# Optimization experiments

Hardware: AMD Instinct MI355X
Metric: run time of the kernel (lower is better)

The kernel has to match this reference:

```python
import jax, jax.numpy as jnp
import numpy as np

N_HEAD = 8
DIM_K = 64
DIM_MODEL = N_HEAD * DIM_K  # 512; must equal seq_len for the final batch_dot
SCALE = DIM_K ** 0.5


def setup_inputs() -> dict:
    key = jax.random.key(0)
    ks = jax.random.split(key, 4)
    B, S, D_IN = 32, 512, 128
    x = jax.random.normal(ks[0], (B, S, D_IN), dtype=jnp.float32)
    init = 0.02
    Wq = jax.random.normal(ks[1], (D_IN * N_HEAD, DIM_MODEL), dtype=jnp.float32) * init
    Wk = jax.random.normal(ks[2], (D_IN * N_HEAD, DIM_MODEL), dtype=jnp.float32) * init
    Wv = jax.random.normal(ks[3], (D_IN * N_HEAD, DIM_MODEL), dtype=jnp.float32) * init
    z = jnp.zeros((DIM_MODEL,), dtype=jnp.float32)
    return {"x": x, "Wq": Wq, "bq": z, "Wk": Wk, "bk": z, "Wv": Wv, "bv": z}


def reference(x, Wq, bq, Wk, bk, Wv, bv):
    # Tile input n_head times along feature dim (matches K.concatenate([q]*n_head))
    xt = jnp.concatenate([x] * N_HEAD, axis=-1)          # [B, S, d_in*n_head]
    q = xt @ Wq + bq                                      # [B, S, dim_model]
    k = xt @ Wk + bk
    v = xt @ Wv + bv
    # K.batch_dot(q, k, axes=[-1,-1]) -> q @ k^T per batch
    scores = jnp.einsum('bsd,btd->bst', q, k) / SCALE     # [B, S, S]
    attn = jax.nn.softmax(scores, axis=-1)
    # K.batch_dot(v, attn, axes=[2,-1]): out[b,i,j] = sum_k v[b,i,k]*attn[b,j,k]
    # (only valid because S == dim_model, as in the original buggy layer)
    out = jnp.einsum('bik,bjk->bij', v, attn)             # [B, S, S]
    return out
```

## Files before the change

### kernel.cpp

```cpp
#include <hip/hip_runtime.h>


typedef unsigned short u16;
typedef __attribute__((ext_vector_type(8))) short bf16x8;
typedef __attribute__((ext_vector_type(4))) float f32x4;
typedef __attribute__((ext_vector_type(2))) float f32x2;
typedef __attribute__((ext_vector_type(2))) unsigned int u32x2;

__device__ inline u16 f2bf(float f) {
  unsigned u = __float_as_uint(f);
  u = u + 0x7fffu + ((u >> 16) & 1u);
  return (u16)(u >> 16);
}
__device__ inline float bf2f(u16 h) { return __uint_as_float(((unsigned)h) << 16); }

__device__ inline void gl16(const u16* g, u16* l) {
  __builtin_amdgcn_global_load_lds(
      (const __attribute__((address_space(1))) unsigned int*)g,
      (__attribute__((address_space(3))) unsigned int*)l, 16, 0, 0);
}

__global__ __launch_bounds__(256)
void prep_w(const float* __restrict__ Wq, const float* __restrict__ Wk,
            const float* __restrict__ Wv,
            u16* __restrict__ WTh, u16* __restrict__ WTl) {
  __shared__ float sm[128][17];
  int t  = blockIdx.x >> 5;
  int nb = blockIdx.x & 31;
  const float* W = (t == 0) ? Wq : (t == 1) ? Wk : Wv;
  int n0 = nb << 4;
  int nl = threadIdx.x & 15;
  int kq = threadIdx.x >> 4;
  float s[8];
#pragma unroll
  for (int i = 0; i < 8; ++i) s[i] = 0.f;
#pragma unroll
  for (int h = 0; h < 8; ++h)
#pragma unroll
    for (int i = 0; i < 8; ++i)
      s[i] += W[(h * 128 + kq + (i << 4)) * 512 + n0 + nl];
#pragma unroll
  for (int i = 0; i < 8; ++i) sm[kq + (i << 4)][nl] = s[i];
  __syncthreads();
  int no = threadIdx.x >> 4;
  int k8 = (threadIdx.x & 15) << 3;
  bf16x8 h8, l8;
#pragma unroll
  for (int c = 0; c < 8; ++c) {
    float v = sm[k8 + c][no];
    u16 h = f2bf(v);
    h8[c] = (short)h;
    l8[c] = (short)f2bf(v - bf2f(h));
  }
  long o = (long)t * 65536 + (long)(n0 + no) * 128 + k8;
  *(bf16x8*)&WTh[o] = h8;
  *(bf16x8*)&WTl[o] = l8;
}

__global__ __launch_bounds__(256)
void split_x(const float* __restrict__ x, u16* __restrict__ xh, u16* __restrict__ xl) {
  int i = blockIdx.x * 256 + threadIdx.x;
  const f32x4* xx = (const f32x4*)x;
  f32x4 a = xx[i * 2], b = xx[i * 2 + 1];
  float v[8] = {a[0], a[1], a[2], a[3], b[0], b[1], b[2], b[3]};
  bf16x8 h8, l8;
#pragma unroll
  for (int j = 0; j < 8; ++j) {
    u16 h = f2bf(v[j]);
    h8[j] = (short)h;
    l8[j] = (short)f2bf(v[j] - bf2f(h));
  }
  ((bf16x8*)xh)[i] = h8;
  ((bf16x8*)xl)[i] = l8;
}

__global__ __launch_bounds__(256, 2)
void proj_fused(const u16* __restrict__ xh, const u16* __restrict__ xl,
                const u16* __restrict__ WTh, const u16* __restrict__ WTl,
                u16* __restrict__ Qh, u16* __restrict__ Kh, u16* __restrict__ Vh,
                const float* __restrict__ bq, const float* __restrict__ bk,
                const float* __restrict__ bv) {
  __shared__ __align__(16) char ldsraw[65536];
  u16* st = (u16*)ldsraw;

  int tid = threadIdx.x;
  int bid = blockIdx.x;
  bid = (bid & 7) * 192 + (bid >> 3);
  int which = bid % 3;
  int tile  = bid / 3;
  int mt = tile >> 2;
  int nt = tile & 3;

  const u16* Ah = xh + (long)mt * (128 * 128);
  const u16* Al = xl + (long)mt * (128 * 128);
  const u16* Bh = WTh + which * 65536 + nt * 16384;
  const u16* Bl = WTl + which * 65536 + nt * 16384;
  const float* bias = (which == 0) ? bq : (which == 1) ? bk : bv;
  u16* C = (which == 0) ? Qh : (which == 1) ? Kh : Vh;

  int lane = tid & 63;
  int wv = tid >> 6;
  int wm = (wv >> 1) << 6;
  int wn = (wv & 1) << 6;
  int frow = lane & 15;
  int fk = (lane >> 4) << 3;

  f32x4 acc[4][4];
#pragma unroll
  for (int i = 0; i < 4; ++i)
#pragma unroll
    for (int j = 0; j < 4; ++j) {
      f32x4 z = {0.f, 0.f, 0.f, 0.f};
      acc[i][j] = z;
    }

  for (int kk = 0; kk < 2; ++kk) {
    int k0 = kk << 6;
#pragma unroll
    for (int j = 0; j < 4; ++j) {
      int c = j * 256 + tid;
      int row = c >> 3;
      int scol = ((c & 7) ^ (row & 7)) << 3;
      int ga = row * 128 + k0 + scol;
      int lo = c << 3;
      gl16(Ah + ga, st + lo);
      gl16(Al + ga, st + 8192 + lo);
      gl16(Bh + ga, st + 16384 + lo);
      gl16(Bl + ga, st + 24576 + lo);
    }
    __syncthreads();
#pragma unroll
    for (int ks = 0; ks < 2; ++ks) {
      int kb = (ks << 5) + fk;
      bf16x8 a_h[4], a_l[4], b_h[4], b_l[4];
#pragma unroll
      for (int i = 0; i < 4; ++i) {
        int ar = wm + (i << 4) + frow;
        int ao = ar * 64 + (kb ^ ((ar & 7) << 3));
        a_h[i] = *(const bf16x8*)&st[ao];
        a_l[i] = *(const bf16x8*)&st[8192 + ao];
        int br = wn + (i << 4) + frow;
        int bo = br * 64 + (kb ^ ((br & 7) << 3));
        b_h[i] = *(const bf16x8*)&st[16384 + bo];
        b_l[i] = *(const bf16x8*)&st[24576 + bo];
      }
#pragma unroll
      for (int i = 0; i < 4; ++i)
#pragma unroll
        for (int j = 0; j < 4; ++j) {
          acc[i][j] = __builtin_amdgcn_mfma_f32_16x16x32_bf16(a_h[i], b_h[j], acc[i][j], 0, 0, 0);
          acc[i][j] = __builtin_amdgcn_mfma_f32_16x16x32_bf16(a_l[i], b_h[j], acc[i][j], 0, 0, 0);
          acc[i][j] = __builtin_amdgcn_mfma_f32_16x16x32_bf16(a_h[i], b_l[j], acc[i][j], 0, 0, 0);
        }
    }
    __syncthreads();
  }

  float* tr = ((float*)ldsraw) + wv * 2112;
  int lr = lane >> 3;
  int c8 = (lane & 7) << 3;
  int colbase = (nt << 7) + wn + c8;
  float bb[8];
#pragma unroll
  for (int c = 0; c < 8; ++c) bb[c] = bias[colbase + c];
  long rowg0 = (long)(mt << 7) + wm;
#pragma unroll
  for (int q = 0; q < 2; ++q) {
#pragma unroll
    for (int il = 0; il < 2; ++il) {
      int i = (q << 1) + il;
#pragma unroll
      for (int j = 0; j < 4; ++j)
#pragma unroll
        for (int r = 0; r < 4; ++r)
          tr[((il << 4) + ((lane >> 4) << 2) + r) * 66 + (j << 4) + (lane & 15)] =
              acc[i][j][r];
    }
#pragma unroll
    for (int p = 0; p < 4; ++p) {
      int rr = (p << 3) + lr;
      float v[8];
      *(f32x2*)&v[0] = *(const f32x2*)&tr[rr * 66 + c8];
      *(f32x2*)&v[2] = *(const f32x2*)&tr[rr * 66 + c8 + 2];
      *(f32x2*)&v[4] = *(const f32x2*)&tr[rr * 66 + c8 + 4];
      *(f32x2*)&v[6] = *(const f32x2*)&tr[rr * 66 + c8 + 6];
      bf16x8 o8;
#pragma unroll
      for (int c = 0; c < 8; ++c) o8[c] = (short)f2bf(v[c] + bb[c]);
      *(bf16x8*)&C[(rowg0 + (q << 5) + rr) * 512 + colbase] = o8;
    }
  }
}

__global__ __launch_bounds__(512, 1)
void attn_fused(const u16* __restrict__ Q, const u16* __restrict__ K,
                const u16* __restrict__ V, float* __restrict__ OUT) {
  __shared__ __align__(16) char LDS[151552];
  u16* B0  = (u16*)LDS;
  u16* B1  = (u16*)(LDS + 32768);
  u16* P16 = (u16*)(LDS + 65536);
  u16* QB0 = (u16*)(LDS + 131072);
  u16* QB1 = (u16*)(LDS + 139264);
  float* smax = (float*)(LDS + 147456);
  float* ssum = (float*)(LDS + 149504);

  int tid = threadIdx.x;
  int p = blockIdx.x;
  int xcd = p & 7, sq = p >> 3;
  int b  = (xcd << 2) + (sq >> 3);
  int jb = sq & 7;

  const u16* Qp = Q + ((long)b * 512 + jb * 64) * 512;
  const u16* Kp = K + (long)b * 262144;
  const u16* Vp = V + (long)b * 262144;

  int lane = tid & 63, nw = tid >> 6;
  int frow = lane & 15, hi4 = lane >> 4;

  auto stageKV = [&](const u16* src, int h, int k0, u16* buf) {
#pragma unroll
    for (int j = 0; j < 4; ++j) {
      int u = (j << 9) + tid;
      int row = u >> 3, slot = u & 7;
      gl16(src + (long)((h << 8) + row) * 512 + k0 + ((slot ^ (row & 7)) << 3),
           buf + (u << 3));
    }
  };
  auto stageQ = [&](int k0, u16* qb) {
    int row = tid >> 3, slot = tid & 7;
    gl16(Qp + (long)row * 512 + k0 + ((slot ^ (row & 7)) << 3), qb + (tid << 3));
  };
  auto rf = [&](const u16* base, int R, int s) -> bf16x8 {
    return *(const bf16x8*)&base[(R << 6) + ((s ^ (R & 7)) << 3)];
  };

  f32x4 acc0[2][4], acc1[2][4];
#pragma unroll
  for (int jj = 0; jj < 2; ++jj)
#pragma unroll
    for (int ii = 0; ii < 4; ++ii) {
      f32x4 z = {0.f, 0.f, 0.f, 0.f};
      acc0[jj][ii] = z;
      acc1[jj][ii] = z;
    }

  stageKV(Kp, 0, 0, B0);
  stageQ(0, QB0);
  __syncthreads();

  for (int k = 0; k < 8; ++k) {
    int k0 = k << 6;
    const u16* qc = (k & 1) ? QB1 : QB0;
    stageKV(Kp, 1, k0, B1);
    {
      bf16x8 af[2][2], qf[2][4];
#pragma unroll
      for (int ks = 0; ks < 2; ++ks) {
#pragma unroll
        for (int jj = 0; jj < 2; ++jj)
          af[ks][jj] = rf(B0, (nw << 5) + (jj << 4) + frow, (ks << 2) + hi4);
#pragma unroll
        for (int ii = 0; ii < 4; ++ii)
          qf[ks][ii] = rf(qc, (ii << 4) + frow, (ks << 2) + hi4);
      }
      __builtin_amdgcn_s_setprio(1);
#pragma unroll
      for (int ks = 0; ks < 2; ++ks)
#pragma unroll
        for (int jj = 0; jj < 2; ++jj)
#pragma unroll
          for (int ii = 0; ii < 4; ++ii)
            acc0[jj][ii] = __builtin_amdgcn_mfma_f32_16x16x32_bf16(af[ks][jj], qf[ks][ii], acc0[jj][ii], 0, 0, 0);
      __builtin_amdgcn_s_setprio(0);
    }
    __syncthreads();
    if (k < 7) { stageKV(Kp, 0, k0 + 64, B0); stageQ(k0 + 64, (k & 1) ? QB0 : QB1); }
    else stageKV(Vp, 0, 0, B0);
    {
      bf16x8 af[2][2], qf[2][4];
#pragma unroll
      for (int ks = 0; ks < 2; ++ks) {
#pragma unroll
        for (int jj = 0; jj < 2; ++jj)
          af[ks][jj] = rf(B1, (nw << 5) + (jj << 4) + frow, (ks << 2) + hi4);
#pragma unroll
        for (int ii = 0; ii < 4; ++ii)
          qf[ks][ii] = rf(qc, (ii << 4) + frow, (ks << 2) + hi4);
      }
      __builtin_amdgcn_s_setprio(1);
#pragma unroll
      for (int ks = 0; ks < 2; ++ks)
#pragma unroll
        for (int jj = 0; jj < 2; ++jj)
#pragma unroll
          for (int ii = 0; ii < 4; ++ii)
            acc1[jj][ii] = __builtin_amdgcn_mfma_f32_16x16x32_bf16(af[ks][jj], qf[ks][ii], acc1[jj][ii], 0, 0, 0);
      __builtin_amdgcn_s_setprio(0);
    }
    if (k < 7) __syncthreads();
  }

  float mx[4], sm[4], inv_[4];
#pragma unroll
  for (int ii = 0; ii < 4; ++ii) {
    float m = acc0[0][ii][0];
#pragma unroll
    for (int jj = 0; jj < 2; ++jj)
#pragma unroll
      for (int r = 0; r < 4; ++r) {
        m = fmaxf(m, acc0[jj][ii][r]);
        m = fmaxf(m, acc1[jj][ii][r]);
      }
    m = fmaxf(m, __shfl_xor(m, 16));
    m = fmaxf(m, __shfl_xor(m, 32));
    mx[ii] = m;
  }
  __syncthreads();
  if (hi4 == 0) {
#pragma unroll
    for (int ii = 0; ii < 4; ++ii) smax[(((ii << 4) + frow) << 3) + nw] = mx[ii];
  }
  __syncthreads();
#pragma unroll
  for (int ii = 0; ii < 4; ++ii) {
    f32x4 a = *(const f32x4*)&smax[((ii << 4) + frow) << 3];
    f32x4 c = *(const f32x4*)&smax[(((ii << 4) + frow) << 3) + 4];
    mx[ii] = fmaxf(fmaxf(fmaxf(a[0], a[1]), fmaxf(a[2], a[3])),
                   fmaxf(fmaxf(c[0], c[1]), fmaxf(c[2], c[3])));
    sm[ii] = 0.f;
  }
#pragma unroll
  for (int jj = 0; jj < 2; ++jj)
#pragma unroll
    for (int ii = 0; ii < 4; ++ii)
#pragma unroll
      for (int r = 0; r < 4; ++r) {
        float p0 = __expf((acc0[jj][ii][r] - mx[ii]) * 0.125f);
        float p1 = __expf((acc1[jj][ii][r] - mx[ii]) * 0.125f);
        acc0[jj][ii][r] = p0;
        acc1[jj][ii][r] = p1;
        sm[ii] += p0 + p1;
      }
#pragma unroll
  for (int ii = 0; ii < 4; ++ii) {
    sm[ii] += __shfl_xor(sm[ii], 16);
    sm[ii] += __shfl_xor(sm[ii], 32);
  }
  if (hi4 == 0) {
#pragma unroll
    for (int ii = 0; ii < 4; ++ii) ssum[(((ii << 4) + frow) << 3) + nw] = sm[ii];
  }
  __syncthreads();
#pragma unroll
  for (int ii = 0; ii < 4; ++ii) {
    f32x4 a = *(const f32x4*)&ssum[((ii << 4) + frow) << 3];
    f32x4 c = *(const f32x4*)&ssum[(((ii << 4) + frow) << 3) + 4];
    inv_[ii] = 1.f / (a[0] + a[1] + a[2] + a[3] + c[0] + c[1] + c[2] + c[3]);
  }
#pragma unroll
  for (int ii = 0; ii < 4; ++ii) {
    int qr = (ii << 4) + frow;
    int rowoff = qr << 10;
    int swz = (qr & 7) << 4;
#pragma unroll
    for (int jj = 0; jj < 2; ++jj) {
      int c0 = ((nw << 5) + (jj << 4) + (hi4 << 2)) << 1;
      unsigned lo0 = (unsigned)f2bf(acc0[jj][ii][0] * inv_[ii]) |
                     ((unsigned)f2bf(acc0[jj][ii][1] * inv_[ii]) << 16);
      unsigned hi0 = (unsigned)f2bf(acc0[jj][ii][2] * inv_[ii]) |
                     ((unsigned)f2bf(acc0[jj][ii][3] * inv_[ii]) << 16);
      u32x2 w0 = {lo0, hi0};
      *(u32x2*)(LDS + 65536 + ((rowoff + c0) ^ swz)) = w0;
      unsigned lo1 = (unsigned)f2bf(acc1[jj][ii][0] * inv_[ii]) |
                     ((unsigned)f2bf(acc1[jj][ii][1] * inv_[ii]) << 16);
      unsigned hi1 = (unsigned)f2bf(acc1[jj][ii][2] * inv_[ii]) |
                     ((unsigned)f2bf(acc1[jj][ii][3] * inv_[ii]) << 16);
      u32x2 w1 = {lo1, hi1};
      *(u32x2*)(LDS + 65536 + ((rowoff + 512 + c0) ^ swz)) = w1;
    }
  }
  __syncthreads();

  f32x4 o0[2][4], o1[2][4];
#pragma unroll
  for (int jj = 0; jj < 2; ++jj)
#pragma unroll
    for (int ii = 0; ii < 4; ++ii) {
      f32x4 z = {0.f, 0.f, 0.f, 0.f};
      o0[jj][ii] = z;
      o1[jj][ii] = z;
    }

  for (int k = 0; k < 8; ++k) {
    int k0 = k << 6;
    stageKV(Vp, 1, k0, B1);
    {
      bf16x8 vf[2][2], pf[2][4];
#pragma unroll
      for (int ks = 0; ks < 2; ++ks) {
#pragma unroll
        for (int jj = 0; jj < 2; ++jj)
          vf[ks][jj] = rf(B0, (nw << 5) + (jj << 4) + frow, (ks << 2) + hi4);
#pragma unroll
        for (int ii = 0; ii < 4; ++ii) {
          int qr = (ii << 4) + frow;
          pf[ks][ii] = *(const bf16x8*)&P16[((qr << 9) + k0 + (ks << 5) + (hi4 << 3)) ^ ((qr & 7) << 3)];
        }
      }
      __builtin_amdgcn_s_setprio(1);
#pragma unroll
      for (int ks = 0; ks < 2; ++ks)
#pragma unroll
        for (int jj = 0; jj < 2; ++jj)
#pragma unroll
          for (int ii = 0; ii < 4; ++ii)
            o0[jj][ii] = __builtin_amdgcn_mfma_f32_16x16x32_bf16(vf[ks][jj], pf[ks][ii], o0[jj][ii], 0, 0, 0);
      __builtin_amdgcn_s_setprio(0);
    }
    __syncthreads();
    if (k < 7) stageKV(Vp, 0, k0 + 64, B0);
    {
      bf16x8 vf[2][2], pf[2][4];
#pragma unroll
      for (int ks = 0; ks < 2; ++ks) {
#pragma unroll
        for (int jj = 0; jj < 2; ++jj)
          vf[ks][jj] = rf(B1, (nw << 5) + (jj << 4) + frow, (ks << 2) + hi4);
#pragma unroll
        for (int ii = 0; ii < 4; ++ii) {
          int qr = (ii << 4) + frow;
          pf[ks][ii] = *(const bf16x8*)&P16[((qr << 9) + k0 + (ks << 5) + (hi4 << 3)) ^ ((qr & 7) << 3)];
        }
      }
      __builtin_amdgcn_s_setprio(1);
#pragma unroll
      for (int ks = 0; ks < 2; ++ks)
#pragma unroll
        for (int jj = 0; jj < 2; ++jj)
#pragma unroll
          for (int ii = 0; ii < 4; ++ii)
            o1[jj][ii] = __builtin_amdgcn_mfma_f32_16x16x32_bf16(vf[ks][jj], pf[ks][ii], o1[jj][ii], 0, 0, 0);
      __builtin_amdgcn_s_setprio(0);
    }
    if (k < 7) __syncthreads();
  }

  float* Ob = OUT + (long)b * 262144 + jb * 64;
#pragma unroll
  for (int jj = 0; jj < 2; ++jj)
#pragma unroll
    for (int ii = 0; ii < 4; ++ii)
#pragma unroll
      for (int r = 0; r < 4; ++r) {
        int vr = (nw << 5) + (jj << 4) + (hi4 << 2) + r;
        int qc = (ii << 4) + frow;
        Ob[(long)vr * 512 + qc] = o0[jj][ii][r];
        Ob[(long)(vr + 256) * 512 + qc] = o1[jj][ii][r];
      }
}

extern "C" void kernel_launch(void* const* d_in, const int* in_sizes, int n_in,
                              void* d_out, int out_size, void* d_ws, size_t ws_size,
                              hipStream_t stream) {
  const float* x  = (const float*)d_in[0];
  const float* Wq = (const float*)d_in[1];
  const float* bq = (const float*)d_in[2];
  const float* Wk = (const float*)d_in[3];
  const float* bk = (const float*)d_in[4];
  const float* Wv = (const float*)d_in[5];
  const float* bv = (const float*)d_in[6];
  float* out = (float*)d_out;

  char* ws = (char*)d_ws;
  size_t off = 0;
  auto alloc = [&](size_t bytes) -> char* {
    char* p = ws + off;
    off = (off + bytes + 255) & ~(size_t)255;
    return p;
  };
  u16* WTh = (u16*)alloc((size_t)3 * 512 * 128 * 2);
  u16* WTl = (u16*)alloc((size_t)3 * 512 * 128 * 2);
  u16* xh  = (u16*)alloc((size_t)16384 * 128 * 2);
  u16* xl  = (u16*)alloc((size_t)16384 * 128 * 2);
  u16* Qh  = (u16*)alloc((size_t)16384 * 512 * 2);
  u16* Kh  = (u16*)alloc((size_t)16384 * 512 * 2);
  u16* Vh  = (u16*)alloc((size_t)16384 * 512 * 2);

  prep_w<<<96, 256, 0, stream>>>(Wq, Wk, Wv, WTh, WTl);
  split_x<<<1024, 256, 0, stream>>>(x, xh, xl);
  proj_fused<<<1536, 256, 0, stream>>>(xh, xl, WTh, WTl, Qh, Kh, Vh, bq, bk, bv);
  attn_fused<<<256, 512, 0, stream>>>(Qh, Kh, Vh, out);
}
```

Before: 82.17 us.

## Preload full Q tile into LDS and use counted vmcnt waits with raw barriers

Loads the block's whole 64x512 Q tile into LDS once at the start, replacing per-step double-buffered Q staging, and reuses that region later for the P matrix. Replaces __syncthreads with explicit s_waitcnt vmcnt(4) plus s_barrier and sched_barrier, so the next K/V tile's loads can stay in flight while the current tile is consumed. Hoists the Q and P fragment reads ahead of the stage issue. The goal is less barrier and full-drain wait overhead and a smaller LDS footprint. The hand-counted vmcnt values and the aliasing of Q with P add correctness risk if the counts or ordering are wrong.

```diff
diff --git a/kernel.cpp b/kernel.cpp
--- a/kernel.cpp
+++ b/kernel.cpp
@@ -19,6 +19,11 @@
       (const __attribute__((address_space(1))) unsigned int*)g,
       (__attribute__((address_space(3))) unsigned int*)l, 16, 0, 0);
 }
+
+#define VM4  asm volatile("s_waitcnt vmcnt(4)" ::: "memory")
+#define VM0  asm volatile("s_waitcnt vmcnt(0)" ::: "memory")
+#define RBAR __builtin_amdgcn_s_barrier()
+#define SB0  __builtin_amdgcn_sched_barrier(0)
 
 __global__ __launch_bounds__(256)
 void prep_w(const float* __restrict__ Wq, const float* __restrict__ Wk,
@@ -195,14 +200,13 @@
 __global__ __launch_bounds__(512, 1)
 void attn_fused(const u16* __restrict__ Q, const u16* __restrict__ K,
                 const u16* __restrict__ V, float* __restrict__ OUT) {
-  __shared__ __align__(16) char LDS[151552];
-  u16* B0  = (u16*)LDS;
-  u16* B1  = (u16*)(LDS + 32768);
-  u16* P16 = (u16*)(LDS + 65536);
-  u16* QB0 = (u16*)(LDS + 131072);
-  u16* QB1 = (u16*)(LDS + 139264);
-  float* smax = (float*)(LDS + 147456);
-  float* ssum = (float*)(LDS + 149504);
+  __shared__ __align__(16) char LDS[135168];
+  u16* QT  = (u16*)LDS;
+  u16* P16 = (u16*)LDS;
+  u16* B0  = (u16*)(LDS + 65536);
+  u16* B1  = (u16*)(LDS + 98304);
+  float* smax = (float*)(LDS + 131072);
+  float* ssum = (float*)(LDS + 133120);
 
   int tid = threadIdx.x;
   int p = blockIdx.x;
@@ -226,12 +230,11 @@
            buf + (u << 3));
     }
   };
-  auto stageQ = [&](int k0, u16* qb) {
-    int row = tid >> 3, slot = tid & 7;
-    gl16(Qp + (long)row * 512 + k0 + ((slot ^ (row & 7)) << 3), qb + (tid << 3));
-  };
   auto rf = [&](const u16* base, int R, int s) -> bf16x8 {
     return *(const bf16x8*)&base[(R << 6) + ((s ^ (R & 7)) << 3)];
+  };
+  auto rq = [&](int row, int s) -> bf16x8 {
+    return *(const bf16x8*)&QT[(row << 9) + ((s ^ (row & 7)) << 3)];
   };
 
   f32x4 acc0[2][4], acc1[2][4];
@@ -244,25 +247,34 @@
       acc1[jj][ii] = z;
     }
 
+#pragma unroll
+  for (int j = 0; j < 8; ++j) {
+    int u = (j << 9) + tid;
+    int row = u >> 6, sl = u & 63;
+    gl16(Qp + (long)row * 512 + ((sl ^ (row & 7)) << 3), QT + (u << 3));
+  }
   stageKV(Kp, 0, 0, B0);
-  stageQ(0, QB0);
-  __syncthreads();
+  VM0;
+  RBAR;
 
   for (int k = 0; k < 8; ++k) {
     int k0 = k << 6;
-    const u16* qc = (k & 1) ? QB1 : QB0;
+    bf16x8 qf[2][4];
+#pragma unroll
+    for (int ks = 0; ks < 2; ++ks)
+#pragma unroll
+      for (int ii = 0; ii < 4; ++ii)
+        qf[ks][ii] = rq((ii << 4) + frow, (k << 3) + (ks << 2) + hi4);
+
     stageKV(Kp, 1, k0, B1);
+    VM4; RBAR; SB0;
     {
-      bf16x8 af[2][2], qf[2][4];
-#pragma unroll
-      for (int ks = 0; ks < 2; ++ks) {
+      bf16x8 af[2][2];
+#pragma unroll
+      for (int ks = 0; ks < 2; ++ks)
 #pragma unroll
         for (int jj = 0; jj < 2; ++jj)
           af[ks][jj] = rf(B0, (nw << 5) + (jj << 4) + frow, (ks << 2) + hi4);
-#pragma unroll
-        for (int ii = 0; ii < 4; ++ii)
-          qf[ks][ii] = rf(qc, (ii << 4) + frow, (ks << 2) + hi4);
-      }
       __builtin_amdgcn_s_setprio(1);
 #pragma unroll
       for (int ks = 0; ks < 2; ++ks)
@@ -273,20 +285,18 @@
             acc0[jj][ii] = __builtin_amdgcn_mfma_f32_16x16x32_bf16(af[ks][jj], qf[ks][ii], acc0[jj][ii], 0, 0, 0);
       __builtin_amdgcn_s_setprio(0);
     }
-    __syncthreads();
-    if (k < 7) { stageKV(Kp, 0, k0 + 64, B0); stageQ(k0 + 64, (k & 1) ? QB0 : QB1); }
-    else stageKV(Vp, 0, 0, B0);
+    RBAR;
+
+    if (k < 7) stageKV(Kp, 0, k0 + 64, B0);
+    else       stageKV(Vp, 0, 0, B0);
+    VM4; RBAR; SB0;
     {
-      bf16x8 af[2][2], qf[2][4];
-#pragma unroll
-      for (int ks = 0; ks < 2; ++ks) {
+      bf16x8 af[2][2];
+#pragma unroll
+      for (int ks = 0; ks < 2; ++ks)
 #pragma unroll
         for (int jj = 0; jj < 2; ++jj)
           af[ks][jj] = rf(B1, (nw << 5) + (jj << 4) + frow, (ks << 2) + hi4);
-#pragma unroll
-        for (int ii = 0; ii < 4; ++ii)
-          qf[ks][ii] = rf(qc, (ii << 4) + frow, (ks << 2) + hi4);
-      }
       __builtin_amdgcn_s_setprio(1);
 #pragma unroll
       for (int ks = 0; ks < 2; ++ks)
@@ -297,7 +307,7 @@
             acc1[jj][ii] = __builtin_amdgcn_mfma_f32_16x16x32_bf16(af[ks][jj], qf[ks][ii], acc1[jj][ii], 0, 0, 0);
       __builtin_amdgcn_s_setprio(0);
     }
-    if (k < 7) __syncthreads();
+    RBAR;
   }
 
   float mx[4], sm[4], inv_[4];
@@ -315,7 +325,6 @@
     m = fmaxf(m, __shfl_xor(m, 32));
     mx[ii] = m;
   }
-  __syncthreads();
   if (hi4 == 0) {
 #pragma unroll
     for (int ii = 0; ii < 4; ++ii) smax[(((ii << 4) + frow) << 3) + nw] = mx[ii];
@@ -370,13 +379,13 @@
       unsigned hi0 = (unsigned)f2bf(acc0[jj][ii][2] * inv_[ii]) |
                      ((unsigned)f2bf(acc0[jj][ii][3] * inv_[ii]) << 16);
       u32x2 w0 = {lo0, hi0};
-      *(u32x2*)(LDS + 65536 + ((rowoff + c0) ^ swz)) = w0;
+      *(u32x2*)(LDS + ((rowoff + c0) ^ swz)) = w0;
       unsigned lo1 = (unsigned)f2bf(acc1[jj][ii][0] * inv_[ii]) |
                      ((unsigned)f2bf(acc1[jj][ii][1] * inv_[ii]) << 16);
       unsigned hi1 = (unsigned)f2bf(acc1[jj][ii][2] * inv_[ii]) |
                      ((unsigned)f2bf(acc1[jj][ii][3] * inv_[ii]) << 16);
       u32x2 w1 = {lo1, hi1};
-      *(u32x2*)(LDS + 65536 + ((rowoff + 512 + c0) ^ swz)) = w1;
+      *(u32x2*)(LDS + ((rowoff + 512 + c0) ^ swz)) = w1;
     }
   }
   __syncthreads();
@@ -393,20 +402,24 @@
 
   for (int k = 0; k < 8; ++k) {
     int k0 = k << 6;
+    bf16x8 pf[2][4];
+#pragma unroll
+    for (int ks = 0; ks < 2; ++ks)
+#pragma unroll
+      for (int ii = 0; ii < 4; ++ii) {
+        int qr = (ii << 4) + frow;
+        pf[ks][ii] = *(const bf16x8*)&P16[((qr << 9) + k0 + (ks << 5) + (hi4 << 3)) ^ ((qr & 7) << 3)];
+      }
+
     stageKV(Vp, 1, k0, B1);
+    VM4; RBAR; SB0;
     {
-      bf16x8 vf[2][2], pf[2][4];
-#pragma unroll
-      for (int ks = 0; ks < 2; ++ks) {
+      bf16x8 vf[2][2];
+#pragma unroll
+      for (int ks = 0; ks < 2; ++ks)
 #pragma unroll
         for (int jj = 0; jj < 2; ++jj)
           vf[ks][jj] = rf(B0, (nw << 5) + (jj << 4) + frow, (ks << 2) + hi4);
-#pragma unroll
-        for (int ii = 0; ii < 4; ++ii) {
-          int qr = (ii << 4) + frow;
-          pf[ks][ii] = *(const bf16x8*)&P16[((qr << 9) + k0 + (ks << 5) + (hi4 << 3)) ^ ((qr & 7) << 3)];
-        }
-      }
       __builtin_amdgcn_s_setprio(1);
 #pragma unroll
       for (int ks = 0; ks < 2; ++ks)
@@ -417,21 +430,18 @@
             o0[jj][ii] = __builtin_amdgcn_mfma_f32_16x16x32_bf16(vf[ks][jj], pf[ks][ii], o0[jj][ii], 0, 0, 0);
       __builtin_amdgcn_s_setprio(0);
     }
-    __syncthreads();
-    if (k < 7) stageKV(Vp, 0, k0 + 64, B0);
+    RBAR;
+
+    if (k < 7) { stageKV(Vp, 0, k0 + 64, B0); VM4; }
+    else VM0;
+    RBAR; SB0;
     {
-      bf16x8 vf[2][2], pf[2][4];
-#pragma unroll
-      for (int ks = 0; ks < 2; ++ks) {
+      bf16x8 vf[2][2];
+#pragma unroll
+      for (int ks = 0; ks < 2; ++ks)
 #pragma unroll
         for (int jj = 0; jj < 2; ++jj)
           vf[ks][jj] = rf(B1, (nw << 5) + (jj << 4) + frow, (ks << 2) + hi4);
-#pragma unroll
-        for (int ii = 0; ii < 4; ++ii) {
-          int qr = (ii << 4) + frow;
-          pf[ks][ii] = *(const bf16x8*)&P16[((qr << 9) + k0 + (ks << 5) + (hi4 << 3)) ^ ((qr & 7) << 3)];
-        }
-      }
       __builtin_amdgcn_s_setprio(1);
 #pragma unroll
       for (int ks = 0; ks < 2; ++ks)
@@ -442,7 +452,7 @@
             o1[jj][ii] = __builtin_amdgcn_mfma_f32_16x16x32_bf16(vf[ks][jj], pf[ks][ii], o1[jj][ii], 0, 0, 0);
       __builtin_amdgcn_s_setprio(0);
     }
-    if (k < 7) __syncthreads();
+    if (k < 7) RBAR;
   }
 
   float* Ob = OUT + (long)b * 262144 + jb * 64;
```

Result: no change. 82.64 us (+0.6%).
